# Performance work log

Hardware: AMD Instinct MI355X
Metric: run time of the kernel (lower is better)

The kernel has to match this reference:

```python
import jax, jax.numpy as jnp
import numpy as np

N = 8192
D_IN = 256
D_OUT = 256


def setup_inputs() -> dict:
    key = jax.random.key(0)
    k1, k2, k3 = jax.random.split(key, 3)
    input = jax.random.normal(k1, (N, D_IN), dtype=jnp.float32)
    adjacencyMatrix = jax.random.uniform(k2, (N, N), dtype=jnp.float32)
    W = jax.random.normal(k3, (D_OUT, D_IN), dtype=jnp.float32) * (1.0 / np.sqrt(D_IN))
    return {"input": input, "adjacencyMatrix": adjacencyMatrix, "W": W}


def reference(input, adjacencyMatrix, W):
    # degree^{-1/2} from row sums
    d_inv_sqrt = jnp.sum(adjacencyMatrix, axis=1) ** -0.5  # [N]
    # D^{-1/2} A D^{-1/2} as row/column scaling (same math as diag matmuls)
    A_norm = adjacencyMatrix * d_inv_sqrt[:, None] * d_inv_sqrt[None, :]  # [N, N]
    # A_norm @ X @ W^T (nn.Linear without bias)
    h = A_norm @ input            # [N, D_IN]
    return h @ W.T                # [N, D_OUT]
```

## Files before the change

kernel.cpp:

```cpp
#include <hip/hip_runtime.h>
#include <stdint.h>

#define NROWS 8192
#define KDIM  8192
#define DIN   256
#define DOUT  256

typedef __attribute__((ext_vector_type(8))) short bf16x8;
typedef __attribute__((ext_vector_type(4))) float f32x4;

__device__ __forceinline__ unsigned short f2bf(float f) {
    union { float f; unsigned u; } v; v.f = f;
    unsigned r = v.u + 0x7FFFu + ((v.u >> 16) & 1u);
    return (unsigned short)(r >> 16);
}

__device__ __forceinline__ void async_load16(const void* g, void* l) {
    __builtin_amdgcn_global_load_lds(
        (__attribute__((address_space(1))) void*)(void*)g,
        (__attribute__((address_space(3))) void*)l, 16, 0, 0);
}

__global__ __launch_bounds__(256) void k_rowsum(const float* __restrict__ A,
                                                float* __restrict__ dis) {
    const int wave = threadIdx.x >> 6, lane = threadIdx.x & 63;
    const int row = (blockIdx.x << 2) + wave;
    const float4* rp = (const float4*)(A + (size_t)row * KDIM);
    float s0 = 0.f, s1 = 0.f, s2 = 0.f, s3 = 0.f;
    #pragma unroll
    for (int it = 0; it < 32; it += 4) {
        float4 v0 = rp[(it + 0) * 64 + lane];
        float4 v1 = rp[(it + 1) * 64 + lane];
        float4 v2 = rp[(it + 2) * 64 + lane];
        float4 v3 = rp[(it + 3) * 64 + lane];
        s0 += (v0.x + v0.y) + (v0.z + v0.w);
        s1 += (v1.x + v1.y) + (v1.z + v1.w);
        s2 += (v2.x + v2.y) + (v2.z + v2.w);
        s3 += (v3.x + v3.y) + (v3.z + v3.w);
    }
    float s = (s0 + s1) + (s2 + s3);
    #pragma unroll
    for (int off = 32; off > 0; off >>= 1) s += __shfl_down(s, off, 64);
    if (lane == 0) dis[row] = rsqrtf(s);
}

__global__ __launch_bounds__(256, 2) void k_xw(const float* __restrict__ X,
                                               const float* __restrict__ W,
                                               const float* __restrict__ dis,
                                               unsigned short* __restrict__ Zst) {
    __shared__ short sX[64 * 72];
    __shared__ short sW[256 * 72];
    __shared__ float disS[64];
    const int tid = threadIdx.x;
    const int w = tid >> 6, lane = tid & 63, lm = lane & 15, lq = lane >> 4;
    const int j0 = blockIdx.x * 64;
    if (tid < 64) disS[tid] = dis[j0 + tid];
    f32x4 acc[4][4] = {};

    for (int s = 0; s < 4; ++s) {
        const int k0 = s * 64;
        #pragma unroll
        for (int i = 0; i < 4; ++i) {
            int e = tid + i * 256;
            int row = e >> 4, c4 = e & 15;
            float4 v = *(const float4*)(X + (size_t)(j0 + row) * DIN + k0 + c4 * 4);
            short4 b; b.x = (short)f2bf(v.x); b.y = (short)f2bf(v.y);
            b.z = (short)f2bf(v.z); b.w = (short)f2bf(v.w);
            *(short4*)&sX[row * 72 + c4 * 4] = b;
        }
        #pragma unroll
        for (int i = 0; i < 16; ++i) {
            int e = tid + i * 256;
            int row = e >> 4, c4 = e & 15;
            float4 v = *(const float4*)(W + (size_t)row * DIN + k0 + c4 * 4);
            short4 b; b.x = (short)f2bf(v.x); b.y = (short)f2bf(v.y);
            b.z = (short)f2bf(v.z); b.w = (short)f2bf(v.w);
            *(short4*)&sW[row * 72 + c4 * 4] = b;
        }
        __syncthreads();
        #pragma unroll
        for (int kk = 0; kk < 2; ++kk) {
            const int koff = kk * 32 + lq * 8;
            bf16x8 a[4], b[4];
            #pragma unroll
            for (int mt = 0; mt < 4; ++mt)
                a[mt] = *(const bf16x8*)&sX[(mt * 16 + lm) * 72 + koff];
            #pragma unroll
            for (int nt = 0; nt < 4; ++nt)
                b[nt] = *(const bf16x8*)&sW[(w * 64 + nt * 16 + lm) * 72 + koff];
            #pragma unroll
            for (int mt = 0; mt < 4; ++mt)
                #pragma unroll
                for (int nt = 0; nt < 4; ++nt)
                    acc[mt][nt] = __builtin_amdgcn_mfma_f32_16x16x32_bf16(
                        a[mt], b[nt], acc[mt][nt], 0, 0, 0);
        }
        __syncthreads();
    }

    #pragma unroll
    for (int mt = 0; mt < 4; ++mt)
        #pragma unroll
        for (int nt = 0; nt < 4; ++nt)
            #pragma unroll
            for (int r = 0; r < 4; ++r) {
                int jl = mt * 16 + lq * 4 + r;
                int n  = w * 64 + nt * 16 + lm;
                float v = acc[mt][nt][r] * disS[jl];
                sW[n * 72 + jl] = (short)f2bf(v);
            }
    __syncthreads();
    #pragma unroll
    for (int it = 0; it < 8; ++it) {
        int e = tid + it * 256;
        int n = e >> 3, ch = e & 7;
        bf16x8 val = *(const bf16x8*)&sW[n * 72 + ch * 8];
        *(bf16x8*)(Zst + (size_t)n * NROWS + j0 + ch * 8) = val;
    }
}

template <bool ATOMIC>
__global__ __launch_bounds__(256, 2) void k_gemm(const float* __restrict__ A,
                                                 const unsigned short* __restrict__ Zst,
                                                 const float* __restrict__ dis,
                                                 float* __restrict__ out) {
    __shared__ short sA[64 * 72];
    __shared__ short sB[256 * 64];
    __shared__ float disS[64];
    const int tid = threadIdx.x;
    const int w = tid >> 6, lane = tid & 63, lm = lane & 15, lq = lane >> 4;
    const int m0 = blockIdx.x * 64;
    const int split = blockIdx.y;
    const int kbase = split * 2048;
    if (tid < 64) disS[tid] = dis[m0 + tid];
    f32x4 acc[4][4] = {};
    short* sBw = &sB[w * 4096];
    const int arow = tid >> 4, ac4 = tid & 15;
    const int swz_c = (lane & 7) ^ (lane >> 3);

    for (int s = 0; s < 32; ++s) {
        const int k0 = kbase + s * 64;
        const unsigned short* gB =
            Zst + (size_t)(w * 64 + (lane >> 3)) * KDIM + k0 + swz_c * 8;
        #pragma unroll
        for (int i = 0; i < 8; ++i)
            async_load16(gB + (size_t)i * 8 * KDIM, &sBw[i * 512]);
        #pragma unroll
        for (int i = 0; i < 4; ++i) {
            int row = arow + i * 16;
            float4 v = *(const float4*)(A + (size_t)(m0 + row) * KDIM + k0 + ac4 * 4);
            short4 b; b.x = (short)f2bf(v.x); b.y = (short)f2bf(v.y);
            b.z = (short)f2bf(v.z); b.w = (short)f2bf(v.w);
            *(short4*)&sA[row * 72 + ac4 * 4] = b;
        }
        __syncthreads();
        #pragma unroll
        for (int kk = 0; kk < 2; ++kk) {
            const int koff = kk * 32 + lq * 8;
            const int cb = kk * 4 + lq;
            bf16x8 a[4], b[4];
            #pragma unroll
            for (int mt = 0; mt < 4; ++mt)
                a[mt] = *(const bf16x8*)&sA[(mt * 16 + lm) * 72 + koff];
            #pragma unroll
            for (int nt = 0; nt < 4; ++nt) {
                int nl = nt * 16 + lm;
                int scb = cb ^ (lm & 7);
                b[nt] = *(const bf16x8*)&sBw[nl * 64 + scb * 8];
            }
            #pragma unroll
            for (int mt = 0; mt < 4; ++mt)
                #pragma unroll
                for (int nt = 0; nt < 4; ++nt)
                    acc[mt][nt] = __builtin_amdgcn_mfma_f32_16x16x32_bf16(
                        a[mt], b[nt], acc[mt][nt], 0, 0, 0);
        }
        __syncthreads();
    }

    #pragma unroll
    for (int mt = 0; mt < 4; ++mt)
        #pragma unroll
        for (int nt = 0; nt < 4; ++nt) {
            int col = w * 64 + nt * 16 + lm;
            #pragma unroll
            for (int r = 0; r < 4; ++r) {
                int rl = mt * 16 + lq * 4 + r;
                float v = acc[mt][nt][r] * disS[rl];
                if (ATOMIC) {
                    atomicAdd(out + (size_t)(m0 + rl) * DOUT + col, v);
                } else {
                    out[(size_t)split * (NROWS * DOUT) + (size_t)(m0 + rl) * DOUT + col] = v;
                }
            }
        }
}

__global__ __launch_bounds__(256) void k_reduce(const float4* __restrict__ p,
                                                float4* __restrict__ out) {
    const size_t i = (size_t)blockIdx.x * 256 + threadIdx.x;
    const size_t stride = (size_t)NROWS * DOUT / 4;
    float4 a = p[i], b = p[i + stride], c = p[i + 2 * stride], d = p[i + 3 * stride];
    float4 r;
    r.x = (a.x + b.x) + (c.x + d.x);
    r.y = (a.y + b.y) + (c.y + d.y);
    r.z = (a.z + b.z) + (c.z + d.z);
    r.w = (a.w + b.w) + (c.w + d.w);
    out[i] = r;
}

extern "C" void kernel_launch(void* const* d_in, const int* in_sizes, int n_in,
                              void* d_out, int out_size, void* d_ws, size_t ws_size,
                              hipStream_t stream) {
    const float* X = (const float*)d_in[0];
    const float* A = (const float*)d_in[1];
    const float* W = (const float*)d_in[2];
    float* out = (float*)d_out;
    char* ws = (char*)d_ws;
    float* dis = (float*)ws;
    unsigned short* Zst = (unsigned short*)(ws + 32768);
    float* part = (float*)(ws + 32768 + 4194304);
    const size_t need = 32768 + 4194304 + 4ull * NROWS * DOUT * sizeof(float);

    k_rowsum<<<NROWS / 4, 256, 0, stream>>>(A, dis);
    k_xw<<<NROWS / 64, 256, 0, stream>>>(X, W, dis, Zst);
    if (ws_size >= need) {
        k_gemm<false><<<dim3(NROWS / 64, 4), 256, 0, stream>>>(A, Zst, dis, part);
        k_reduce<<<(NROWS * DOUT / 4) / 256, 256, 0, stream>>>((const float4*)part,
                                                               (float4*)out);
    } else {
        hipMemsetAsync(d_out, 0, (size_t)out_size * sizeof(float), stream);
        k_gemm<true><<<dim3(NROWS / 64, 4), 256, 0, stream>>>(A, Zst, dis, out);
    }
}
```

Before: 451.4 us.

## Pre-convert adjacency to bf16 in rowsum pass and stream it asynchronously in GEMM

The row-sum kernel now also writes a bf16 copy of the adjacency matrix into workspace. The main GEMM then loads A tiles with async global-to-LDS loads using the same XOR swizzle as the B operand, replacing the per-iteration fp32 register loads and in-loop conversion. This removes conversion ALU work and register staging from the GEMM loop and halves the bytes the GEMM reads for A. In exchange it adds a 128MB write plus read of the bf16 copy and needs a much larger workspace; if the workspace is too small, the code falls back to the atomic fp32 path.

```diff
diff --git a/kernel.cpp b/kernel.cpp
--- a/kernel.cpp
+++ b/kernel.cpp
@@ -21,24 +21,29 @@
         (__attribute__((address_space(3))) void*)l, 16, 0, 0);
 }
 
-__global__ __launch_bounds__(256) void k_rowsum(const float* __restrict__ A,
-                                                float* __restrict__ dis) {
+__global__ __launch_bounds__(256) void k_rowsum_cvt(const float* __restrict__ A,
+                                                    float* __restrict__ dis,
+                                                    unsigned short* __restrict__ Abf) {
     const int wave = threadIdx.x >> 6, lane = threadIdx.x & 63;
     const int row = (blockIdx.x << 2) + wave;
     const float4* rp = (const float4*)(A + (size_t)row * KDIM);
-    float s0 = 0.f, s1 = 0.f, s2 = 0.f, s3 = 0.f;
-    #pragma unroll
-    for (int it = 0; it < 32; it += 4) {
+    short4* wp = (short4*)(Abf + (size_t)row * KDIM);
+    float s0 = 0.f, s1 = 0.f;
+    #pragma unroll
+    for (int it = 0; it < 32; it += 2) {
         float4 v0 = rp[(it + 0) * 64 + lane];
         float4 v1 = rp[(it + 1) * 64 + lane];
-        float4 v2 = rp[(it + 2) * 64 + lane];
-        float4 v3 = rp[(it + 3) * 64 + lane];
+        short4 b0, b1;
+        b0.x = (short)f2bf(v0.x); b0.y = (short)f2bf(v0.y);
+        b0.z = (short)f2bf(v0.z); b0.w = (short)f2bf(v0.w);
+        b1.x = (short)f2bf(v1.x); b1.y = (short)f2bf(v1.y);
+        b1.z = (short)f2bf(v1.z); b1.w = (short)f2bf(v1.w);
+        wp[(it + 0) * 64 + lane] = b0;
+        wp[(it + 1) * 64 + lane] = b1;
         s0 += (v0.x + v0.y) + (v0.z + v0.w);
         s1 += (v1.x + v1.y) + (v1.z + v1.w);
-        s2 += (v2.x + v2.y) + (v2.z + v2.w);
-        s3 += (v3.x + v3.y) + (v3.z + v3.w);
-    }
-    float s = (s0 + s1) + (s2 + s3);
+    }
+    float s = s0 + s1;
     #pragma unroll
     for (int off = 32; off > 0; off >>= 1) s += __shfl_down(s, off, 64);
     if (lane == 0) dis[row] = rsqrtf(s);
@@ -119,11 +124,76 @@
     }
 }
 
-template <bool ATOMIC>
-__global__ __launch_bounds__(256, 2) void k_gemm(const float* __restrict__ A,
-                                                 const unsigned short* __restrict__ Zst,
-                                                 const float* __restrict__ dis,
-                                                 float* __restrict__ out) {
+__global__ __launch_bounds__(256, 2) void k_gemm_bf(const unsigned short* __restrict__ Abf,
+                                                    const unsigned short* __restrict__ Zst,
+                                                    const float* __restrict__ dis,
+                                                    float* __restrict__ part) {
+    __shared__ short sA[64 * 64];
+    __shared__ short sB[256 * 64];
+    __shared__ float disS[64];
+    const int tid = threadIdx.x;
+    const int w = tid >> 6, lane = tid & 63, lm = lane & 15, lq = lane >> 4;
+    const int m0 = blockIdx.x * 64;
+    const int split = blockIdx.y;
+    const int kbase = split * 2048;
+    if (tid < 64) disS[tid] = dis[m0 + tid];
+    f32x4 acc[4][4] = {};
+    short* sAw = &sA[w * 1024];
+    short* sBw = &sB[w * 4096];
+    const int swz = (lane & 7) ^ (lane >> 3);
+    const unsigned short* gA =
+        Abf + (size_t)(m0 + w * 16 + (lane >> 3)) * KDIM + kbase + swz * 8;
+    const unsigned short* gB =
+        Zst + (size_t)(w * 64 + (lane >> 3)) * KDIM + kbase + swz * 8;
+
+    for (int s = 0; s < 32; ++s) {
+        const int kofs = s * 64;
+        #pragma unroll
+        for (int i = 0; i < 2; ++i)
+            async_load16(gA + kofs + (size_t)i * 8 * KDIM, &sAw[i * 512]);
+        #pragma unroll
+        for (int i = 0; i < 8; ++i)
+            async_load16(gB + kofs + (size_t)i * 8 * KDIM, &sBw[i * 512]);
+        __syncthreads();
+        #pragma unroll
+        for (int kk = 0; kk < 2; ++kk) {
+            const int cb = kk * 4 + lq;
+            const int scb = cb ^ (lm & 7);
+            bf16x8 a[4], b[4];
+            #pragma unroll
+            for (int mt = 0; mt < 4; ++mt)
+                a[mt] = *(const bf16x8*)&sA[(mt * 16 + lm) * 64 + scb * 8];
+            #pragma unroll
+            for (int nt = 0; nt < 4; ++nt)
+                b[nt] = *(const bf16x8*)&sBw[(nt * 16 + lm) * 64 + scb * 8];
+            #pragma unroll
+            for (int mt = 0; mt < 4; ++mt)
+                #pragma unroll
+                for (int nt = 0; nt < 4; ++nt)
+                    acc[mt][nt] = __builtin_amdgcn_mfma_f32_16x16x32_bf16(
+                        a[mt], b[nt], acc[mt][nt], 0, 0, 0);
+        }
+        __syncthreads();
+    }
+
+    #pragma unroll
+    for (int mt = 0; mt < 4; ++mt)
+        #pragma unroll
+        for (int nt = 0; nt < 4; ++nt) {
+            int col = w * 64 + nt * 16 + lm;
+            #pragma unroll
+            for (int r = 0; r < 4; ++r) {
+                int rl = mt * 16 + lq * 4 + r;
+                float v = acc[mt][nt][r] * disS[rl];
+                part[(size_t)split * (NROWS * DOUT) + (size_t)(m0 + rl) * DOUT + col] = v;
+            }
+        }
+}
+
+__global__ __launch_bounds__(256, 2) void k_gemm_f32(const float* __restrict__ A,
+                                                     const unsigned short* __restrict__ Zst,
+                                                     const float* __restrict__ dis,
+                                                     float* __restrict__ out) {
     __shared__ short sA[64 * 72];
     __shared__ short sB[256 * 64];
     __shared__ float disS[64];
@@ -136,12 +206,12 @@
     f32x4 acc[4][4] = {};
     short* sBw = &sB[w * 4096];
     const int arow = tid >> 4, ac4 = tid & 15;
-    const int swz_c = (lane & 7) ^ (lane >> 3);
+    const int swz = (lane & 7) ^ (lane >> 3);
 
     for (int s = 0; s < 32; ++s) {
         const int k0 = kbase + s * 64;
         const unsigned short* gB =
-            Zst + (size_t)(w * 64 + (lane >> 3)) * KDIM + k0 + swz_c * 8;
+            Zst + (size_t)(w * 64 + (lane >> 3)) * KDIM + k0 + swz * 8;
         #pragma unroll
         for (int i = 0; i < 8; ++i)
             async_load16(gB + (size_t)i * 8 * KDIM, &sBw[i * 512]);
@@ -158,16 +228,14 @@
         for (int kk = 0; kk < 2; ++kk) {
             const int koff = kk * 32 + lq * 8;
             const int cb = kk * 4 + lq;
+            const int scb = cb ^ (lm & 7);
             bf16x8 a[4], b[4];
             #pragma unroll
             for (int mt = 0; mt < 4; ++mt)
                 a[mt] = *(const bf16x8*)&sA[(mt * 16 + lm) * 72 + koff];
             #pragma unroll
-            for (int nt = 0; nt < 4; ++nt) {
-                int nl = nt * 16 + lm;
-                int scb = cb ^ (lm & 7);
-                b[nt] = *(const bf16x8*)&sBw[nl * 64 + scb * 8];
-            }
+            for (int nt = 0; nt < 4; ++nt)
+                b[nt] = *(const bf16x8*)&sBw[(nt * 16 + lm) * 64 + scb * 8];
             #pragma unroll
             for (int mt = 0; mt < 4; ++mt)
                 #pragma unroll
@@ -177,7 +245,6 @@
         }
         __syncthreads();
     }
-
     #pragma unroll
     for (int mt = 0; mt < 4; ++mt)
         #pragma unroll
@@ -186,12 +253,8 @@
             #pragma unroll
             for (int r = 0; r < 4; ++r) {
                 int rl = mt * 16 + lq * 4 + r;
-                float v = acc[mt][nt][r] * disS[rl];
-                if (ATOMIC) {
-                    atomicAdd(out + (size_t)(m0 + rl) * DOUT + col, v);
-                } else {
-                    out[(size_t)split * (NROWS * DOUT) + (size_t)(m0 + rl) * DOUT + col] = v;
-                }
+                atomicAdd(out + (size_t)(m0 + rl) * DOUT + col,
+                          acc[mt][nt][r] * disS[rl]);
             }
         }
 }
@@ -209,6 +272,25 @@
     out[i] = r;
 }
 
+__global__ __launch_bounds__(256) void k_rowsum(const float* __restrict__ A,
+                                                float* __restrict__ dis) {
+    const int wave = threadIdx.x >> 6, lane = threadIdx.x & 63;
+    const int row = (blockIdx.x << 2) + wave;
+    const float4* rp = (const float4*)(A + (size_t)row * KDIM);
+    float s0 = 0.f, s1 = 0.f;
+    #pragma unroll
+    for (int it = 0; it < 32; it += 2) {
+        float4 v0 = rp[(it + 0) * 64 + lane];
+        float4 v1 = rp[(it + 1) * 64 + lane];
+        s0 += (v0.x + v0.y) + (v0.z + v0.w);
+        s1 += (v1.x + v1.y) + (v1.z + v1.w);
+    }
+    float s = s0 + s1;
+    #pragma unroll
+    for (int off = 32; off > 0; off >>= 1) s += __shfl_down(s, off, 64);
+    if (lane == 0) dis[row] = rsqrtf(s);
+}
+
 extern "C" void kernel_launch(void* const* d_in, const int* in_sizes, int n_in,
                               void* d_out, int out_size, void* d_ws, size_t ws_size,
                               hipStream_t stream) {
@@ -219,17 +301,22 @@
     char* ws = (char*)d_ws;
     float* dis = (float*)ws;
     unsigned short* Zst = (unsigned short*)(ws + 32768);
-    float* part = (float*)(ws + 32768 + 4194304);
-    const size_t need = 32768 + 4194304 + 4ull * NROWS * DOUT * sizeof(float);
-
-    k_rowsum<<<NROWS / 4, 256, 0, stream>>>(A, dis);
-    k_xw<<<NROWS / 64, 256, 0, stream>>>(X, W, dis, Zst);
-    if (ws_size >= need) {
-        k_gemm<false><<<dim3(NROWS / 64, 4), 256, 0, stream>>>(A, Zst, dis, part);
+    unsigned short* Abf = (unsigned short*)(ws + 32768 + (4 << 20));
+    float* part = (float*)(ws + 32768 + (4 << 20) + (128ull << 20));
+    const size_t need_full = 32768 + (4ull << 20) + (128ull << 20) +
+                             4ull * NROWS * DOUT * sizeof(float);
+    const size_t need_min = 32768 + (4ull << 20);
+
+    if (ws_size >= need_full) {
+        k_rowsum_cvt<<<NROWS / 4, 256, 0, stream>>>(A, dis, Abf);
+        k_xw<<<NROWS / 64, 256, 0, stream>>>(X, W, dis, Zst);
+        k_gemm_bf<<<dim3(NROWS / 64, 4), 256, 0, stream>>>(Abf, Zst, dis, part);
         k_reduce<<<(NROWS * DOUT / 4) / 256, 256, 0, stream>>>((const float4*)part,
                                                                (float4*)out);
-    } else {
+    } else if (ws_size >= need_min) {
+        k_rowsum<<<NROWS / 4, 256, 0, stream>>>(A, dis);
+        k_xw<<<NROWS / 64, 256, 0, stream>>>(X, W, dis, Zst);
         hipMemsetAsync(d_out, 0, (size_t)out_size * sizeof(float), stream);
-        k_gemm<true><<<dim3(NROWS / 64, 4), 256, 0, stream>>>(A, Zst, dis, out);
-    }
-}
+        k_gemm_f32<<<dim3(NROWS / 64, 4), 256, 0, stream>>>(A, Zst, dis, out);
+    }
+}
```

Result: slower. 465.5 us (+3.1%).
